# Kernel tuning notes

Hardware: AMD Instinct MI355X
Metric: run time of the kernel (lower is better)

## Reference

```python
import jax, jax.numpy as jnp
import numpy as np

B, S, P, I = 32, 64, 32, 256
NF, H, L = 4, 512, 2
OUT = 2
INITRANGE = 0.1
assert NF * I == 2 * H  # layer-2 GRU input dim equals layer-1 input dim


def setup_inputs() -> dict:
    key = jax.random.key(0)
    ks = jax.random.split(key, 12)
    u = lambda k, shape: jax.random.uniform(k, shape, jnp.float32, -INITRANGE, INITRANGE)
    return {
        "inputs": jax.random.normal(ks[0], (B, S, P, I), jnp.float32),
        "inputs_demoip": jax.random.normal(ks[1], (B, 3), jnp.float32),
        "conv_w": u(ks[2], (NF, I)),            # Conv1d(1, NF, kernel=I) == dot product
        "conv_b": u(ks[3], (NF,)),
        "conv2_w": u(ks[4], (2 * H,)),          # Conv1d(1, 1, kernel=2H) == dot product
        "conv2_b": u(ks[5], (1,)),
        "wih": u(ks[6], (L, 2, 3 * H, NF * I)),  # [layer, dir, 3H, in]
        "whh": u(ks[7], (L, 2, 3 * H, H)),
        "bih": u(ks[8], (L, 2, 3 * H)),
        "bhh": u(ks[9], (L, 2, 3 * H)),
        "lin_w": u(ks[10], (OUT, 2 * H + 3)),
        "lin_b": u(ks[11], (OUT,)),
        "batch_size": B,
    }


def _gru_dir(x, wih, whh, bih, bhh, reverse):
    """One direction of a torch-style GRU. x: [B,S,in] -> [B,S,H]."""
    gx = jnp.einsum('bsi,gi->bsg', x, wih) + bih  # precompute input gates [B,S,3H]
    if reverse:
        gx = gx[:, ::-1]
    h0 = jnp.zeros((x.shape[0], H), x.dtype)

    def step(h, gxt):
        gh = h @ whh.T + bhh
        xr, xz, xn = jnp.split(gxt, 3, axis=-1)
        hr, hz, hn = jnp.split(gh, 3, axis=-1)
        r = jax.nn.sigmoid(xr + hr)
        z = jax.nn.sigmoid(xz + hz)
        n = jnp.tanh(xn + r * hn)
        h_new = (1.0 - z) * n + z * h
        return h_new, h_new

    _, ys = jax.lax.scan(step, h0, gx.transpose(1, 0, 2))
    ys = ys.transpose(1, 0, 2)  # [B,S,H]
    if reverse:
        ys = ys[:, ::-1]
    return ys


def reference(inputs, inputs_demoip, conv_w, conv_b, conv2_w, conv2_b,
              wih, whh, bih, bhh, lin_w, lin_b, batch_size):
    # --- convolutional attention embedding (kernel spans full input -> dot product) ---
    scores = jnp.einsum('bspi,fi->bsfp', inputs, conv_w) + conv_b[None, None, :, None]
    conv_wts = jax.nn.softmax(scores, axis=-1)                    # softmax over pad dim
    vec = jnp.einsum('bsfp,bspi->bsfi', conv_wts, inputs)         # [B,S,NF,I]
    embedding = vec.reshape(batch_size, S, NF * I)                # [B,S,NF*I]

    # --- stacked bidirectional GRU (eval mode: dropout omitted) ---
    x = embedding
    for l in range(L):
        f = _gru_dir(x, wih[l, 0], whh[l, 0], bih[l, 0], bhh[l, 0], False)
        b = _gru_dir(x, wih[l, 1], whh[l, 1], bih[l, 1], bhh[l, 1], True)
        x = jnp.concatenate([f, b], axis=-1)
    states = x                                                    # [B,S,2H]

    # --- second attention (conv2 kernel spans 2H -> dot product per step) ---
    alpha = jax.nn.softmax(states @ conv2_w + conv2_b[0], axis=1)  # [B,S]
    context = jnp.einsum('bs,bsh->bh', alpha, states)              # [B,2H]

    context_v2 = jnp.concatenate([context, inputs_demoip], axis=1)  # [B,2H+3]
    out = jax.nn.softmax(context_v2 @ lin_w.T + lin_b, axis=1)      # [B,OUT]
    return out, conv_wts, states, context, alpha
```

## Files before the change

### kernel.cpp

```cpp
#include <hip/hip_runtime.h>

typedef __attribute__((ext_vector_type(8))) short s8v;
typedef __attribute__((ext_vector_type(8))) __bf16 bf8v;
typedef __attribute__((ext_vector_type(4))) float f32x4;
typedef unsigned long long ULL;

#define DEVINL __device__ __forceinline__

DEVINL unsigned short f2bf(float f) {
    unsigned int x = __float_as_uint(f);
    unsigned int r = (x + 0x7FFFu + ((x >> 16) & 1u)) >> 16;
    return (unsigned short)r;
}

DEVINL f32x4 mfma16(s8v a, s8v b, f32x4 c) {
    return __builtin_amdgcn_mfma_f32_16x16x32_bf16(
        __builtin_bit_cast(bf8v, a), __builtin_bit_cast(bf8v, b), c, 0, 0, 0);
}

typedef const __attribute__((address_space(1))) unsigned int gu32;
typedef __attribute__((address_space(3))) unsigned int lu32;
DEVINL void gload16(const void* g, unsigned int lds_off) {
    __builtin_amdgcn_global_load_lds((gu32*)g, (lu32*)(size_t)lds_off, 16, 0, 0);
}

#define WS_CTR   0
#define WS_HBUF  4096
#define WS_ZERO_BYTES 266240
#define WS_WIH   266240
#define WS_WHH   (WS_WIH + 12582912)
#define WS_EMB   (WS_WHH + 6291456)
#define WS_ST1   (WS_EMB + 4194304)
#define WS_GX    (WS_ST1 + 4194304)

__global__ __launch_bounds__(256) void k_cvt(const float* __restrict__ in,
                                             unsigned short* __restrict__ out, int n) {
    int i0 = (blockIdx.x * 256 + threadIdx.x) * 8;
    if (i0 + 8 > n) return;
    f32x4 a = *(const f32x4*)(in + i0);
    f32x4 b = *(const f32x4*)(in + i0 + 4);
    s8v o;
    o[0] = (short)f2bf(a[0]); o[1] = (short)f2bf(a[1]);
    o[2] = (short)f2bf(a[2]); o[3] = (short)f2bf(a[3]);
    o[4] = (short)f2bf(b[0]); o[5] = (short)f2bf(b[1]);
    o[6] = (short)f2bf(b[2]); o[7] = (short)f2bf(b[3]);
    *(s8v*)(out + i0) = o;
}

__global__ __launch_bounds__(256) void k_conv(const float* __restrict__ inp,
                                              const float* __restrict__ conv_w,
                                              const float* __restrict__ conv_b,
                                              float* __restrict__ wts_out,
                                              unsigned short* __restrict__ emb) {
    const int bs = blockIdx.x, tid = threadIdx.x;
    __shared__ float xs[32][260];
    __shared__ float sc[4][32];
    __shared__ float wts[4][32];
    const float* x = inp + (size_t)bs * 8192;
    {
        int p = tid >> 3, i0 = (tid & 7) * 32;
        const float* src = x + p * 256 + i0;
        float* dst = &xs[p][i0];
#pragma unroll
        for (int j = 0; j < 32; j += 4) *(f32x4*)(dst + j) = *(const f32x4*)(src + j);
    }
    __syncthreads();
    {
        int p = tid >> 3, o = tid & 7;
        float s0 = 0, s1 = 0, s2 = 0, s3 = 0;
        const float* xp = &xs[p][o * 32];
#pragma unroll
        for (int j = 0; j < 32; j += 4) {
            f32x4 v  = *(const f32x4*)(xp + j);
            f32x4 w0 = *(const f32x4*)(conv_w + o * 32 + j);
            f32x4 w1 = *(const f32x4*)(conv_w + 256 + o * 32 + j);
            f32x4 w2 = *(const f32x4*)(conv_w + 512 + o * 32 + j);
            f32x4 w3 = *(const f32x4*)(conv_w + 768 + o * 32 + j);
#pragma unroll
            for (int q = 0; q < 4; ++q) {
                s0 += v[q] * w0[q]; s1 += v[q] * w1[q];
                s2 += v[q] * w2[q]; s3 += v[q] * w3[q];
            }
        }
#pragma unroll
        for (int d = 4; d; d >>= 1) {
            s0 += __shfl_down(s0, d, 8); s1 += __shfl_down(s1, d, 8);
            s2 += __shfl_down(s2, d, 8); s3 += __shfl_down(s3, d, 8);
        }
        if (o == 0) {
            sc[0][p] = s0 + conv_b[0]; sc[1][p] = s1 + conv_b[1];
            sc[2][p] = s2 + conv_b[2]; sc[3][p] = s3 + conv_b[3];
        }
    }
    __syncthreads();
    if (tid < 4) {
        float mx = -1e30f;
        for (int p = 0; p < 32; ++p) mx = fmaxf(mx, sc[tid][p]);
        float sm = 0.f;
        for (int p = 0; p < 32; ++p) { float e = __expf(sc[tid][p] - mx); wts[tid][p] = e; sm += e; }
        float inv = 1.f / sm;
        for (int p = 0; p < 32; ++p) wts[tid][p] *= inv;
    }
    __syncthreads();
    if (tid < 128) wts_out[(size_t)bs * 128 + tid] = wts[tid >> 5][tid & 31];
    {
        float a0 = 0, a1 = 0, a2 = 0, a3 = 0;
#pragma unroll 8
        for (int p = 0; p < 32; ++p) {
            float v = xs[p][tid];
            a0 += wts[0][p] * v; a1 += wts[1][p] * v;
            a2 += wts[2][p] * v; a3 += wts[3][p] * v;
        }
        unsigned short* e = emb + (size_t)bs * 1024;
        e[tid] = f2bf(a0); e[256 + tid] = f2bf(a1);
        e[512 + tid] = f2bf(a2); e[768 + tid] = f2bf(a3);
    }
}

__global__ __launch_bounds__(256, 2) void k_gemm(const unsigned short* __restrict__ A,
                                                 const unsigned short* __restrict__ B,
                                                 const float* __restrict__ bias,
                                                 const float* __restrict__ bias2,
                                                 float* __restrict__ C,
                                                 int M, int N, int K) {
    const int bm = blockIdx.y * 128, bn = blockIdx.x * 64;
    const int tid = threadIdx.x, w = tid >> 6, l = tid & 63;
    const int wr = w >> 1, wc = w & 1;
    const int lr = l & 15, lq = l >> 4;

    __shared__ __align__(1024) unsigned short As[8192];
    __shared__ __align__(1024) unsigned short Bs[4096];
    const unsigned int AsOff = (unsigned int)(size_t)(void*)As;
    const unsigned int BsOff = (unsigned int)(size_t)(void*)Bs;

    f32x4 acc[4][2] = {};
    const int srow = tid >> 3;
    const int scol = ((tid & 7) ^ (srow & 7)) * 8;
    const unsigned int wbase = w * 1024;

    for (int k0 = 0; k0 < K; k0 += 64) {
        __syncthreads();
#pragma unroll
        for (int j = 0; j < 4; ++j)
            gload16(A + (size_t)(bm + j * 32 + srow) * K + k0 + scol,
                    AsOff + j * 4096 + wbase);
#pragma unroll
        for (int j = 0; j < 2; ++j)
            gload16(B + (size_t)(bn + j * 32 + srow) * K + k0 + scol,
                    BsOff + j * 4096 + wbase);
        asm volatile("s_waitcnt vmcnt(0)" ::: "memory");
        __syncthreads();
#pragma unroll
        for (int kk = 0; kk < 2; ++kk) {
            s8v af[4], bf_[2];
#pragma unroll
            for (int mt = 0; mt < 4; ++mt) {
                const int row = wr * 64 + mt * 16 + lr;
                const int qg = kk * 4 + lq;
                af[mt] = *(const s8v*)((const char*)As + row * 128 +
                                       ((qg ^ (row & 7)) << 4));
            }
#pragma unroll
            for (int nt = 0; nt < 2; ++nt) {
                const int row = wc * 32 + nt * 16 + lr;
                const int qg = kk * 4 + lq;
                bf_[nt] = *(const s8v*)((const char*)Bs + row * 128 +
                                        ((qg ^ (row & 7)) << 4));
            }
#pragma unroll
            for (int mt = 0; mt < 4; ++mt)
#pragma unroll
                for (int nt = 0; nt < 2; ++nt)
                    acc[mt][nt] = mfma16(af[mt], bf_[nt], acc[mt][nt]);
        }
    }
#pragma unroll
    for (int mt = 0; mt < 4; ++mt)
#pragma unroll
        for (int nt = 0; nt < 2; ++nt)
#pragma unroll
            for (int r = 0; r < 4; ++r) {
                int row = bm + wr * 64 + mt * 16 + lq * 4 + r;
                int col = bn + wc * 32 + nt * 16 + lr;
                int gg = col >> 9;
                float b2 = (gg != 2 && gg != 5) ? bias2[col] : 0.f;
                C[(size_t)row * N + col] = acc[mt][nt][r] + bias[col] + b2;
            }
}

__global__ __launch_bounds__(256, 1) void k_scan(const float* __restrict__ gx,
                                                 const unsigned short* __restrict__ whh,
                                                 const float* __restrict__ bhh,
                                                 unsigned short* __restrict__ hbuf,
                                                 unsigned int* __restrict__ flags,
                                                 float* __restrict__ st32,
                                                 unsigned short* __restrict__ st16) {
    const int blk = blockIdx.x;
    const int dir = blk >> 3, jg = blk & 7;
    const int tid = threadIdx.x;
    const int w = tid >> 6, l = tid & 63;
    const int lr = l & 15, lq = l >> 4;
    const int jb = jg * 64;
    const int mycol = jb + w * 16 + lr;

    __shared__ __align__(1024) unsigned short hs[16384];

    s8v bf[3][16];
#pragma unroll
    for (int g = 0; g < 3; ++g) {
        const unsigned short* wr =
            whh + ((size_t)dir * 1536 + g * 512 + mycol) * 512 + lq * 8;
#pragma unroll
        for (int kt = 0; kt < 16; ++kt) bf[g][kt] = *(const s8v*)(wr + kt * 32);
    }
    const float bh_n = bhh[dir * 1536 + 1024 + mycol];

    unsigned short* hb0 = hbuf + (size_t)dir * 32768;
    unsigned int* fl = flags + dir * 128;
    unsigned int* myflag = fl + jg * 16;

    float hp[2][4] = {{0.f, 0.f, 0.f, 0.f}, {0.f, 0.f, 0.f, 0.f}};

    for (int t = 0; t < 64; ++t) {
        const int s = dir ? (63 - t) : t;
        float pg[3][2][4];
#pragma unroll
        for (int g = 0; g < 3; ++g)
#pragma unroll
            for (int bt = 0; bt < 2; ++bt)
#pragma unroll
                for (int r = 0; r < 4; ++r) {
                    const int b = bt * 16 + lq * 4 + r;
                    pg[g][bt][r] = gx[(size_t)(b * 64 + s) * 3072 + dir * 1536 +
                                      g * 512 + mycol];
                }
        if (t > 0) {
            for (;;) {
                bool ok = (l >= 8) ||
                          (__hip_atomic_load(&fl[l * 16], __ATOMIC_RELAXED,
                                             __HIP_MEMORY_SCOPE_AGENT) >= (unsigned)t);
                if (__all(ok)) break;
                __builtin_amdgcn_s_sleep(1);
            }
        }
        const unsigned short* hc = hb0 + (size_t)(t & 1) * 16384;
#pragma unroll
        for (int i = 0; i < 8; ++i) {
            const int c = tid + 256 * i;
            const int row = c >> 6, inb = (c & 63) * 16;
            const ULL* hq = (const ULL*)(hc + c * 8);
            ULL d0 = __hip_atomic_load(hq, __ATOMIC_RELAXED, __HIP_MEMORY_SCOPE_AGENT);
            ULL d1 = __hip_atomic_load(hq + 1, __ATOMIC_RELAXED, __HIP_MEMORY_SCOPE_AGENT);
            char* dst = (char*)hs + row * 1024 + (inb ^ ((row & 7) << 4));
            *(ULL*)dst = d0;
            *(ULL*)(dst + 8) = d1;
        }
        __syncthreads();
        f32x4 acc[3][2] = {};
#pragma unroll
        for (int bt = 0; bt < 2; ++bt) {
            const int row = bt * 16 + lr;
            const int m = (row & 7) << 4;
#pragma unroll
            for (int kt = 0; kt < 16; ++kt) {
                s8v a = *(const s8v*)((const char*)hs + row * 1024 +
                                      ((kt * 64 + lq * 16) ^ m));
                acc[0][bt] = mfma16(a, bf[0][kt], acc[0][bt]);
                acc[1][bt] = mfma16(a, bf[1][kt], acc[1][bt]);
                acc[2][bt] = mfma16(a, bf[2][kt], acc[2][bt]);
            }
        }
        unsigned short* hnw = hb0 + (size_t)((t + 1) & 1) * 16384;
        float hnew[2][4];
#pragma unroll
        for (int bt = 0; bt < 2; ++bt)
#pragma unroll
            for (int r = 0; r < 4; ++r) {
                const int b = bt * 16 + lq * 4 + r;
                float r_ = __builtin_amdgcn_rcpf(
                    1.f + __expf(-(pg[0][bt][r] + acc[0][bt][r])));
                float z_ = __builtin_amdgcn_rcpf(
                    1.f + __expf(-(pg[1][bt][r] + acc[1][bt][r])));
                float q = pg[2][bt][r] + r_ * (acc[2][bt][r] + bh_n);
                q = fminf(fmaxf(q, -15.f), 15.f);
                float e = __expf(2.f * q);
                float n_ = (e - 1.f) * __builtin_amdgcn_rcpf(e + 1.f);
                float h = (1.f - z_) * n_ + z_ * hp[bt][r];
                hp[bt][r] = h;
                hnew[bt][r] = h;
                __hip_atomic_store(&hnw[b * 512 + mycol], f2bf(h), __ATOMIC_RELAXED,
                                   __HIP_MEMORY_SCOPE_AGENT);
            }
        __syncthreads();
        if (tid == 0 && t < 63)
            __hip_atomic_store(myflag, (unsigned)(t + 1), __ATOMIC_RELAXED,
                               __HIP_MEMORY_SCOPE_AGENT);
#pragma unroll
        for (int bt = 0; bt < 2; ++bt)
#pragma unroll
            for (int r = 0; r < 4; ++r) {
                const int b = bt * 16 + lq * 4 + r;
                const size_t so = (size_t)(b * 64 + s) * 1024 + dir * 512 + mycol;
                if (st32) st32[so] = hnew[bt][r];
                if (st16) st16[so] = f2bf(hnew[bt][r]);
            }
    }
}

__global__ __launch_bounds__(256) void k_finale(const float* __restrict__ states,
                                                const float* __restrict__ conv2_w,
                                                const float* __restrict__ conv2_b,
                                                const float* __restrict__ demoip,
                                                const float* __restrict__ lin_w,
                                                const float* __restrict__ lin_b,
                                                float* __restrict__ out,
                                                float* __restrict__ context,
                                                float* __restrict__ alpha) {
    const int b = blockIdx.x, tid = threadIdx.x, w = tid >> 6, l = tid & 63;
    __shared__ float dots[64], al[64], ctx[1024], lg[2];
    const float* st = states + (size_t)b * 65536;
    for (int si = 0; si < 16; ++si) {
        int s = w * 16 + si;
        const float* row = st + s * 1024;
        float sum = 0.f;
        for (int i = l; i < 1024; i += 64) sum += row[i] * conv2_w[i];
#pragma unroll
        for (int m = 32; m; m >>= 1) sum += __shfl_xor(sum, m, 64);
        if (l == 0) dots[s] = sum + conv2_b[0];
    }
    __syncthreads();
    if (w == 0) {
        float v = dots[l];
        float mx = v;
#pragma unroll
        for (int m = 32; m; m >>= 1) mx = fmaxf(mx, __shfl_xor(mx, m, 64));
        float e = __expf(v - mx);
        float sm = e;
#pragma unroll
        for (int m = 32; m; m >>= 1) sm += __shfl_xor(sm, m, 64);
        float a = e / sm;
        al[l] = a;
        alpha[b * 64 + l] = a;
    }
    __syncthreads();
    for (int h = tid; h < 1024; h += 256) {
        float c = 0.f;
#pragma unroll 8
        for (int s = 0; s < 64; ++s) c += al[s] * st[s * 1024 + h];
        ctx[h] = c;
        context[b * 1024 + h] = c;
    }
    __syncthreads();
    if (w < 2) {
        const float* lw = lin_w + w * 1027;
        float sum = 0.f;
        for (int i = l; i < 1024; i += 64) sum += ctx[i] * lw[i];
#pragma unroll
        for (int m = 32; m; m >>= 1) sum += __shfl_xor(sum, m, 64);
        if (l == 0) {
            sum += lw[1024] * demoip[b * 3] + lw[1025] * demoip[b * 3 + 1] +
                   lw[1026] * demoip[b * 3 + 2] + lin_b[w];
            lg[w] = sum;
        }
    }
    __syncthreads();
    if (tid == 0) {
        float m = fmaxf(lg[0], lg[1]);
        float e0 = __expf(lg[0] - m), e1 = __expf(lg[1] - m);
        float inv = 1.f / (e0 + e1);
        out[b * 2 + 0] = e0 * inv;
        out[b * 2 + 1] = e1 * inv;
    }
}

extern "C" void kernel_launch(void* const* d_in, const int* in_sizes, int n_in,
                              void* d_out, int out_size, void* d_ws, size_t ws_size,
                              hipStream_t stream) {
    const float* inputs  = (const float*)d_in[0];
    const float* demoip  = (const float*)d_in[1];
    const float* conv_w  = (const float*)d_in[2];
    const float* conv_b  = (const float*)d_in[3];
    const float* conv2_w = (const float*)d_in[4];
    const float* conv2_b = (const float*)d_in[5];
    const float* wih     = (const float*)d_in[6];
    const float* whh     = (const float*)d_in[7];
    const float* bih     = (const float*)d_in[8];
    const float* bhh     = (const float*)d_in[9];
    const float* lin_w   = (const float*)d_in[10];
    const float* lin_b   = (const float*)d_in[11];

    char* ws = (char*)d_ws;
    unsigned int* ctrs    = (unsigned int*)(ws + WS_CTR);
    unsigned short* hbuf  = (unsigned short*)(ws + WS_HBUF);
    unsigned short* wih16 = (unsigned short*)(ws + WS_WIH);
    unsigned short* whh16 = (unsigned short*)(ws + WS_WHH);
    unsigned short* emb16 = (unsigned short*)(ws + WS_EMB);
    unsigned short* st116 = (unsigned short*)(ws + WS_ST1);
    float* gxbuf          = (float*)(ws + WS_GX);

    float* out_out    = (float*)d_out;
    float* wts_out    = out_out + 64;
    float* states_out = out_out + 262208;
    float* ctx_out    = out_out + 2359360;
    float* alpha_out  = out_out + 2392128;

    hipMemsetAsync(ws, 0, WS_ZERO_BYTES, stream);
    k_cvt<<<3072, 256, 0, stream>>>(wih, wih16, 6291456);
    k_cvt<<<1536, 256, 0, stream>>>(whh, whh16, 3145728);
    k_conv<<<2048, 256, 0, stream>>>(inputs, conv_w, conv_b, wts_out, emb16);
    k_gemm<<<dim3(48, 16), 256, 0, stream>>>(emb16, wih16, bih, bhh, gxbuf,
                                             2048, 3072, 1024);
    k_scan<<<16, 256, 0, stream>>>(gxbuf, whh16, bhh, hbuf, ctrs, nullptr, st116);
    k_gemm<<<dim3(48, 16), 256, 0, stream>>>(st116, wih16 + 3145728, bih + 3072,
                                             bhh + 3072, gxbuf, 2048, 3072, 1024);
    k_scan<<<16, 256, 0, stream>>>(gxbuf, whh16 + 1572864, bhh + 3072, hbuf + 65536,
                                   ctrs + 256, states_out, nullptr);
    k_finale<<<32, 256, 0, stream>>>(states_out, conv2_w, conv2_b, demoip, lin_w, lin_b,
                                     out_out, ctx_out, alpha_out);
}
```

Measured before the change: 834.1 us.

## Fuse both GRU layers' GEMMs and scans into one persistent producer-consumer kernel

Replaces the four separate GEMM and scan launches with one persistent kernel of 256 blocks. Sixteen blocks run the recurrent scan and the other 240 compute input-gate GEMM tiles, publishing per-column-tile completion counters. Each scan block starts as soon as the gate columns it needs are complete, rather than waiting for the whole GEMM kernel to finish, and the layer-2 GEMM starts once a done counter shows every layer-1 scan block has finished. The per-step flag wait is also changed so one wave polls and then releases the block through a barrier. The design depends on all 256 blocks being resident at once and on relaxed atomic loads and stores for cross-block visibility, which adds deadlock and memory-ordering risk.

```diff
diff --git a/kernel.cpp b/kernel.cpp
--- a/kernel.cpp
+++ b/kernel.cpp
@@ -24,10 +24,24 @@
     __builtin_amdgcn_global_load_lds((gu32*)g, (lu32*)(size_t)lds_off, 16, 0, 0);
 }
 
+#define AGENT __HIP_MEMORY_SCOPE_AGENT
+DEVINL unsigned int aload(const unsigned int* p) {
+    return __hip_atomic_load(p, __ATOMIC_RELAXED, AGENT);
+}
+DEVINL float aloadf(const float* p) {
+    return __hip_atomic_load(p, __ATOMIC_RELAXED, AGENT);
+}
+DEVINL ULL aload8(const ULL* p) {
+    return __hip_atomic_load(p, __ATOMIC_RELAXED, AGENT);
+}
+
 #define WS_CTR   0
-#define WS_HBUF  4096
-#define WS_ZERO_BYTES 266240
-#define WS_WIH   266240
+#define WS_GC1   4096
+#define WS_GC2   7168
+#define WS_DONE  10240
+#define WS_HBUF  10496
+#define WS_ZERO_BYTES 272640
+#define WS_WIH   272640
 #define WS_WHH   (WS_WIH + 12582912)
 #define WS_EMB   (WS_WHH + 6291456)
 #define WS_ST1   (WS_EMB + 4194304)
@@ -117,19 +131,19 @@
     }
 }
 
-__global__ __launch_bounds__(256, 2) void k_gemm(const unsigned short* __restrict__ A,
-                                                 const unsigned short* __restrict__ B,
-                                                 const float* __restrict__ bias,
-                                                 const float* __restrict__ bias2,
-                                                 float* __restrict__ C,
-                                                 int M, int N, int K) {
-    const int bm = blockIdx.y * 128, bn = blockIdx.x * 64;
-    const int tid = threadIdx.x, w = tid >> 6, l = tid & 63;
+DEVINL void do_tile(const unsigned short* __restrict__ A,
+                    const unsigned short* __restrict__ B,
+                    const float* __restrict__ bias,
+                    const float* __restrict__ bias2,
+                    float* __restrict__ C,
+                    unsigned int* __restrict__ gcnt,
+                    int id, int tid, char* smem) {
+    const int bm = (id & 15) * 128, bn = (id >> 4) * 64;
+    const int w = tid >> 6, l = tid & 63;
     const int wr = w >> 1, wc = w & 1;
     const int lr = l & 15, lq = l >> 4;
-
-    __shared__ __align__(1024) unsigned short As[8192];
-    __shared__ __align__(1024) unsigned short Bs[4096];
+    unsigned short* As = (unsigned short*)smem;
+    unsigned short* Bs = (unsigned short*)(smem + 16384);
     const unsigned int AsOff = (unsigned int)(size_t)(void*)As;
     const unsigned int BsOff = (unsigned int)(size_t)(void*)Bs;
 
@@ -138,15 +152,15 @@
     const int scol = ((tid & 7) ^ (srow & 7)) * 8;
     const unsigned int wbase = w * 1024;
 
-    for (int k0 = 0; k0 < K; k0 += 64) {
+    for (int k0 = 0; k0 < 1024; k0 += 64) {
         __syncthreads();
 #pragma unroll
         for (int j = 0; j < 4; ++j)
-            gload16(A + (size_t)(bm + j * 32 + srow) * K + k0 + scol,
+            gload16(A + (size_t)(bm + j * 32 + srow) * 1024 + k0 + scol,
                     AsOff + j * 4096 + wbase);
 #pragma unroll
         for (int j = 0; j < 2; ++j)
-            gload16(B + (size_t)(bn + j * 32 + srow) * K + k0 + scol,
+            gload16(B + (size_t)(bn + j * 32 + srow) * 1024 + k0 + scol,
                     BsOff + j * 4096 + wbase);
         asm volatile("s_waitcnt vmcnt(0)" ::: "memory");
         __syncthreads();
@@ -184,39 +198,49 @@
                 int col = bn + wc * 32 + nt * 16 + lr;
                 int gg = col >> 9;
                 float b2 = (gg != 2 && gg != 5) ? bias2[col] : 0.f;
-                C[(size_t)row * N + col] = acc[mt][nt][r] + bias[col] + b2;
-            }
-}
-
-__global__ __launch_bounds__(256, 1) void k_scan(const float* __restrict__ gx,
-                                                 const unsigned short* __restrict__ whh,
-                                                 const float* __restrict__ bhh,
-                                                 unsigned short* __restrict__ hbuf,
-                                                 unsigned int* __restrict__ flags,
-                                                 float* __restrict__ st32,
-                                                 unsigned short* __restrict__ st16) {
-    const int blk = blockIdx.x;
-    const int dir = blk >> 3, jg = blk & 7;
-    const int tid = threadIdx.x;
+                float v = acc[mt][nt][r] + bias[col] + b2;
+                __hip_atomic_store(&C[(size_t)row * 3072 + col], v,
+                                   __ATOMIC_RELAXED, AGENT);
+            }
+    __syncthreads();
+    if (tid == 0)
+        (void)__hip_atomic_fetch_add(&gcnt[(id >> 4) * 16], 1u, __ATOMIC_RELAXED, AGENT);
+}
+
+DEVINL void scan_layer(int dir, int jg, int tid,
+                       const float* __restrict__ gx,
+                       const unsigned short* __restrict__ whh_l,
+                       const float* __restrict__ bhh_l,
+                       unsigned short* __restrict__ hbuf_l,
+                       unsigned int* __restrict__ fl_base,
+                       unsigned int* __restrict__ gcnt,
+                       float* __restrict__ st32,
+                       unsigned short* __restrict__ st16,
+                       unsigned short* __restrict__ hs) {
     const int w = tid >> 6, l = tid & 63;
     const int lr = l & 15, lq = l >> 4;
     const int jb = jg * 64;
     const int mycol = jb + w * 16 + lr;
 
-    __shared__ __align__(1024) unsigned short hs[16384];
+    for (;;) {
+        bool ok = true;
+        if (l < 3) ok = aload(&gcnt[(dir * 24 + l * 8 + jg) * 16]) >= 16u;
+        if (__all(ok)) break;
+        __builtin_amdgcn_s_sleep(4);
+    }
 
     s8v bf[3][16];
 #pragma unroll
     for (int g = 0; g < 3; ++g) {
         const unsigned short* wr =
-            whh + ((size_t)dir * 1536 + g * 512 + mycol) * 512 + lq * 8;
+            whh_l + ((size_t)dir * 1536 + g * 512 + mycol) * 512 + lq * 8;
 #pragma unroll
         for (int kt = 0; kt < 16; ++kt) bf[g][kt] = *(const s8v*)(wr + kt * 32);
     }
-    const float bh_n = bhh[dir * 1536 + 1024 + mycol];
-
-    unsigned short* hb0 = hbuf + (size_t)dir * 32768;
-    unsigned int* fl = flags + dir * 128;
+    const float bh_n = bhh_l[dir * 1536 + 1024 + mycol];
+
+    unsigned short* hb0 = hbuf_l + (size_t)dir * 32768;
+    unsigned int* fl = fl_base + dir * 128;
     unsigned int* myflag = fl + jg * 16;
 
     float hp[2][4] = {{0.f, 0.f, 0.f, 0.f}, {0.f, 0.f, 0.f, 0.f}};
@@ -231,17 +255,14 @@
 #pragma unroll
                 for (int r = 0; r < 4; ++r) {
                     const int b = bt * 16 + lq * 4 + r;
-                    pg[g][bt][r] = gx[(size_t)(b * 64 + s) * 3072 + dir * 1536 +
-                                      g * 512 + mycol];
+                    pg[g][bt][r] = aloadf(&gx[(size_t)(b * 64 + s) * 3072 +
+                                              dir * 1536 + g * 512 + mycol]);
                 }
         if (t > 0) {
-            for (;;) {
-                bool ok = (l >= 8) ||
-                          (__hip_atomic_load(&fl[l * 16], __ATOMIC_RELAXED,
-                                             __HIP_MEMORY_SCOPE_AGENT) >= (unsigned)t);
-                if (__all(ok)) break;
-                __builtin_amdgcn_s_sleep(1);
-            }
+            if (w == 0 && l < 8) {
+                while (aload(&fl[l * 16]) < (unsigned)t) __builtin_amdgcn_s_sleep(1);
+            }
+            __syncthreads();
         }
         const unsigned short* hc = hb0 + (size_t)(t & 1) * 16384;
 #pragma unroll
@@ -249,8 +270,8 @@
             const int c = tid + 256 * i;
             const int row = c >> 6, inb = (c & 63) * 16;
             const ULL* hq = (const ULL*)(hc + c * 8);
-            ULL d0 = __hip_atomic_load(hq, __ATOMIC_RELAXED, __HIP_MEMORY_SCOPE_AGENT);
-            ULL d1 = __hip_atomic_load(hq + 1, __ATOMIC_RELAXED, __HIP_MEMORY_SCOPE_AGENT);
+            ULL d0 = aload8(hq);
+            ULL d1 = aload8(hq + 1);
             char* dst = (char*)hs + row * 1024 + (inb ^ ((row & 7) << 4));
             *(ULL*)dst = d0;
             *(ULL*)(dst + 8) = d1;
@@ -289,12 +310,11 @@
                 hp[bt][r] = h;
                 hnew[bt][r] = h;
                 __hip_atomic_store(&hnw[b * 512 + mycol], f2bf(h), __ATOMIC_RELAXED,
-                                   __HIP_MEMORY_SCOPE_AGENT);
+                                   AGENT);
             }
         __syncthreads();
         if (tid == 0 && t < 63)
-            __hip_atomic_store(myflag, (unsigned)(t + 1), __ATOMIC_RELAXED,
-                               __HIP_MEMORY_SCOPE_AGENT);
+            __hip_atomic_store(myflag, (unsigned)(t + 1), __ATOMIC_RELAXED, AGENT);
 #pragma unroll
         for (int bt = 0; bt < 2; ++bt)
 #pragma unroll
@@ -302,8 +322,46 @@
                 const int b = bt * 16 + lq * 4 + r;
                 const size_t so = (size_t)(b * 64 + s) * 1024 + dir * 512 + mycol;
                 if (st32) st32[so] = hnew[bt][r];
-                if (st16) st16[so] = f2bf(hnew[bt][r]);
-            }
+                if (st16)
+                    __hip_atomic_store(&st16[so], f2bf(hnew[bt][r]), __ATOMIC_RELAXED,
+                                       AGENT);
+            }
+    }
+}
+
+__global__ __launch_bounds__(256, 1) void k_mega(
+    const unsigned short* __restrict__ emb16,
+    const unsigned short* __restrict__ wih16,
+    const float* __restrict__ bih,
+    const float* __restrict__ bhh,
+    float* __restrict__ gx,
+    const unsigned short* __restrict__ whh16,
+    unsigned short* __restrict__ st116,
+    float* __restrict__ states_out,
+    unsigned short* __restrict__ hbuf,
+    unsigned int* __restrict__ flags,
+    unsigned int* __restrict__ gc1,
+    unsigned int* __restrict__ gc2,
+    unsigned int* __restrict__ done) {
+    __shared__ __align__(1024) char smem[32768];
+    const int blk = blockIdx.x, tid = threadIdx.x;
+    if (blk < 16) {
+        const int dir = blk >> 3, jg = blk & 7;
+        scan_layer(dir, jg, tid, gx, whh16, bhh, hbuf, flags, gc1,
+                   nullptr, st116, (unsigned short*)smem);
+        __syncthreads();
+        if (tid == 0)
+            (void)__hip_atomic_fetch_add(done, 1u, __ATOMIC_RELAXED, AGENT);
+        scan_layer(dir, jg, tid, gx, whh16 + 1572864, bhh + 3072, hbuf + 65536,
+                   flags + 256, gc2, states_out, nullptr, (unsigned short*)smem);
+    } else {
+        const int wid = blk - 16;
+        for (int id = wid; id < 768; id += 240)
+            do_tile(emb16, wih16, bih, bhh, gx, gc1, id, tid, smem);
+        while (aload(done) < 16u) __builtin_amdgcn_s_sleep(16);
+        for (int id = wid; id < 768; id += 240)
+            do_tile(st116, wih16 + 3145728, bih + 3072, bhh + 3072, gx, gc2, id, tid,
+                    smem);
     }
 }
 
@@ -390,7 +448,10 @@
     const float* lin_b   = (const float*)d_in[11];
 
     char* ws = (char*)d_ws;
-    unsigned int* ctrs    = (unsigned int*)(ws + WS_CTR);
+    unsigned int* flags   = (unsigned int*)(ws + WS_CTR);
+    unsigned int* gc1     = (unsigned int*)(ws + WS_GC1);
+    unsigned int* gc2     = (unsigned int*)(ws + WS_GC2);
+    unsigned int* done    = (unsigned int*)(ws + WS_DONE);
     unsigned short* hbuf  = (unsigned short*)(ws + WS_HBUF);
     unsigned short* wih16 = (unsigned short*)(ws + WS_WIH);
     unsigned short* whh16 = (unsigned short*)(ws + WS_WHH);
@@ -408,13 +469,8 @@
     k_cvt<<<3072, 256, 0, stream>>>(wih, wih16, 6291456);
     k_cvt<<<1536, 256, 0, stream>>>(whh, whh16, 3145728);
     k_conv<<<2048, 256, 0, stream>>>(inputs, conv_w, conv_b, wts_out, emb16);
-    k_gemm<<<dim3(48, 16), 256, 0, stream>>>(emb16, wih16, bih, bhh, gxbuf,
-                                             2048, 3072, 1024);
-    k_scan<<<16, 256, 0, stream>>>(gxbuf, whh16, bhh, hbuf, ctrs, nullptr, st116);
-    k_gemm<<<dim3(48, 16), 256, 0, stream>>>(st116, wih16 + 3145728, bih + 3072,
-                                             bhh + 3072, gxbuf, 2048, 3072, 1024);
-    k_scan<<<16, 256, 0, stream>>>(gxbuf, whh16 + 1572864, bhh + 3072, hbuf + 65536,
-                                   ctrs + 256, states_out, nullptr);
+    k_mega<<<256, 256, 0, stream>>>(emb16, wih16, bih, bhh, gxbuf, whh16, st116,
+                                    states_out, hbuf, flags, gc1, gc2, done);
     k_finale<<<32, 256, 0, stream>>>(states_out, conv2_w, conv2_b, demoip, lin_w, lin_b,
                                      out_out, ctx_out, alpha_out);
 }
```

New measurement: 1.002 ms. 1.2x slower.

## Merge weight conversion, conv and flag reset into one prep kernel; simplify scan wait

Applied to the files above, without the earlier changes.

Folds the two bf16 weight-conversion launches, the conv attention kernel and the workspace memset into a single k_prep launch. Block 0 of that launch zeroes the flag counters. In the scan, a single wave now spins on the flags and then releases the block with a barrier, and the step-0 h-load and MFMA work are skipped because h is zero. This cuts launch and memset overhead and per-step polling traffic, at the cost of an extra barrier per step. The hbuf region is no longer zeroed, which is safe only because the t==0 path never reads it.

```diff
diff --git a/kernel.cpp b/kernel.cpp
--- a/kernel.cpp
+++ b/kernel.cpp
@@ -24,35 +24,48 @@
     __builtin_amdgcn_global_load_lds((gu32*)g, (lu32*)(size_t)lds_off, 16, 0, 0);
 }
 
+#define AGENT __HIP_MEMORY_SCOPE_AGENT
+
 #define WS_CTR   0
 #define WS_HBUF  4096
-#define WS_ZERO_BYTES 266240
 #define WS_WIH   266240
 #define WS_WHH   (WS_WIH + 12582912)
 #define WS_EMB   (WS_WHH + 6291456)
 #define WS_ST1   (WS_EMB + 4194304)
 #define WS_GX    (WS_ST1 + 4194304)
 
-__global__ __launch_bounds__(256) void k_cvt(const float* __restrict__ in,
-                                             unsigned short* __restrict__ out, int n) {
-    int i0 = (blockIdx.x * 256 + threadIdx.x) * 8;
-    if (i0 + 8 > n) return;
-    f32x4 a = *(const f32x4*)(in + i0);
-    f32x4 b = *(const f32x4*)(in + i0 + 4);
-    s8v o;
-    o[0] = (short)f2bf(a[0]); o[1] = (short)f2bf(a[1]);
-    o[2] = (short)f2bf(a[2]); o[3] = (short)f2bf(a[3]);
-    o[4] = (short)f2bf(b[0]); o[5] = (short)f2bf(b[1]);
-    o[6] = (short)f2bf(b[2]); o[7] = (short)f2bf(b[3]);
-    *(s8v*)(out + i0) = o;
-}
-
-__global__ __launch_bounds__(256) void k_conv(const float* __restrict__ inp,
+__global__ __launch_bounds__(256) void k_prep(const float* __restrict__ inp,
                                               const float* __restrict__ conv_w,
                                               const float* __restrict__ conv_b,
                                               float* __restrict__ wts_out,
-                                              unsigned short* __restrict__ emb) {
-    const int bs = blockIdx.x, tid = threadIdx.x;
+                                              unsigned short* __restrict__ emb,
+                                              const float* __restrict__ wih,
+                                              unsigned short* __restrict__ wih16,
+                                              const float* __restrict__ whh,
+                                              unsigned short* __restrict__ whh16,
+                                              unsigned int* __restrict__ flagz) {
+    const int bid = blockIdx.x, tid = threadIdx.x;
+    if (bid >= 2048) {
+        const float* src;
+        unsigned short* dst;
+        int i0;
+        if (bid < 5120) { src = wih; dst = wih16; i0 = ((bid - 2048) * 256 + tid) * 8; }
+        else            { src = whh; dst = whh16; i0 = ((bid - 5120) * 256 + tid) * 8; }
+        f32x4 a = *(const f32x4*)(src + i0);
+        f32x4 b = *(const f32x4*)(src + i0 + 4);
+        s8v o;
+        o[0] = (short)f2bf(a[0]); o[1] = (short)f2bf(a[1]);
+        o[2] = (short)f2bf(a[2]); o[3] = (short)f2bf(a[3]);
+        o[4] = (short)f2bf(b[0]); o[5] = (short)f2bf(b[1]);
+        o[6] = (short)f2bf(b[2]); o[7] = (short)f2bf(b[3]);
+        *(s8v*)(dst + i0) = o;
+        return;
+    }
+    const int bs = bid;
+    if (bs == 0) {
+        for (int i = tid; i < 1024; i += 256)
+            __hip_atomic_store(&flagz[i], 0u, __ATOMIC_RELAXED, AGENT);
+    }
     __shared__ float xs[32][260];
     __shared__ float sc[4][32];
     __shared__ float wts[4][32];
@@ -234,40 +247,39 @@
                     pg[g][bt][r] = gx[(size_t)(b * 64 + s) * 3072 + dir * 1536 +
                                       g * 512 + mycol];
                 }
+        f32x4 acc[3][2] = {};
         if (t > 0) {
-            for (;;) {
-                bool ok = (l >= 8) ||
-                          (__hip_atomic_load(&fl[l * 16], __ATOMIC_RELAXED,
-                                             __HIP_MEMORY_SCOPE_AGENT) >= (unsigned)t);
-                if (__all(ok)) break;
-                __builtin_amdgcn_s_sleep(1);
-            }
-        }
-        const unsigned short* hc = hb0 + (size_t)(t & 1) * 16384;
-#pragma unroll
-        for (int i = 0; i < 8; ++i) {
-            const int c = tid + 256 * i;
-            const int row = c >> 6, inb = (c & 63) * 16;
-            const ULL* hq = (const ULL*)(hc + c * 8);
-            ULL d0 = __hip_atomic_load(hq, __ATOMIC_RELAXED, __HIP_MEMORY_SCOPE_AGENT);
-            ULL d1 = __hip_atomic_load(hq + 1, __ATOMIC_RELAXED, __HIP_MEMORY_SCOPE_AGENT);
-            char* dst = (char*)hs + row * 1024 + (inb ^ ((row & 7) << 4));
-            *(ULL*)dst = d0;
-            *(ULL*)(dst + 8) = d1;
-        }
-        __syncthreads();
-        f32x4 acc[3][2] = {};
-#pragma unroll
-        for (int bt = 0; bt < 2; ++bt) {
-            const int row = bt * 16 + lr;
-            const int m = (row & 7) << 4;
-#pragma unroll
-            for (int kt = 0; kt < 16; ++kt) {
-                s8v a = *(const s8v*)((const char*)hs + row * 1024 +
-                                      ((kt * 64 + lq * 16) ^ m));
-                acc[0][bt] = mfma16(a, bf[0][kt], acc[0][bt]);
-                acc[1][bt] = mfma16(a, bf[1][kt], acc[1][bt]);
-                acc[2][bt] = mfma16(a, bf[2][kt], acc[2][bt]);
+            if (w == 0 && l < 8) {
+                while (__hip_atomic_load(&fl[l * 16], __ATOMIC_RELAXED, AGENT) <
+                       (unsigned)t)
+                    __builtin_amdgcn_s_sleep(1);
+            }
+            __syncthreads();
+            const unsigned short* hc = hb0 + (size_t)(t & 1) * 16384;
+#pragma unroll
+            for (int i = 0; i < 8; ++i) {
+                const int c = tid + 256 * i;
+                const int row = c >> 6, inb = (c & 63) * 16;
+                const ULL* hq = (const ULL*)(hc + c * 8);
+                ULL d0 = __hip_atomic_load(hq, __ATOMIC_RELAXED, AGENT);
+                ULL d1 = __hip_atomic_load(hq + 1, __ATOMIC_RELAXED, AGENT);
+                char* dst = (char*)hs + row * 1024 + (inb ^ ((row & 7) << 4));
+                *(ULL*)dst = d0;
+                *(ULL*)(dst + 8) = d1;
+            }
+            __syncthreads();
+#pragma unroll
+            for (int bt = 0; bt < 2; ++bt) {
+                const int row = bt * 16 + lr;
+                const int m = (row & 7) << 4;
+#pragma unroll
+                for (int kt = 0; kt < 16; ++kt) {
+                    s8v a = *(const s8v*)((const char*)hs + row * 1024 +
+                                          ((kt * 64 + lq * 16) ^ m));
+                    acc[0][bt] = mfma16(a, bf[0][kt], acc[0][bt]);
+                    acc[1][bt] = mfma16(a, bf[1][kt], acc[1][bt]);
+                    acc[2][bt] = mfma16(a, bf[2][kt], acc[2][bt]);
+                }
             }
         }
         unsigned short* hnw = hb0 + (size_t)((t + 1) & 1) * 16384;
@@ -289,12 +301,11 @@
                 hp[bt][r] = h;
                 hnew[bt][r] = h;
                 __hip_atomic_store(&hnw[b * 512 + mycol], f2bf(h), __ATOMIC_RELAXED,
-                                   __HIP_MEMORY_SCOPE_AGENT);
+                                   AGENT);
             }
         __syncthreads();
         if (tid == 0 && t < 63)
-            __hip_atomic_store(myflag, (unsigned)(t + 1), __ATOMIC_RELAXED,
-                               __HIP_MEMORY_SCOPE_AGENT);
+            __hip_atomic_store(myflag, (unsigned)(t + 1), __ATOMIC_RELAXED, AGENT);
 #pragma unroll
         for (int bt = 0; bt < 2; ++bt)
 #pragma unroll
@@ -404,10 +415,8 @@
     float* ctx_out    = out_out + 2359360;
     float* alpha_out  = out_out + 2392128;
 
-    hipMemsetAsync(ws, 0, WS_ZERO_BYTES, stream);
-    k_cvt<<<3072, 256, 0, stream>>>(wih, wih16, 6291456);
-    k_cvt<<<1536, 256, 0, stream>>>(whh, whh16, 3145728);
-    k_conv<<<2048, 256, 0, stream>>>(inputs, conv_w, conv_b, wts_out, emb16);
+    k_prep<<<6656, 256, 0, stream>>>(inputs, conv_w, conv_b, wts_out, emb16,
+                                     wih, wih16, whh, whh16, ctrs);
     k_gemm<<<dim3(48, 16), 256, 0, stream>>>(emb16, wih16, bih, bhh, gxbuf,
                                              2048, 3072, 1024);
     k_scan<<<16, 256, 0, stream>>>(gxbuf, whh16, bhh, hbuf, ctrs, nullptr, st116);
```

Result: faster. 801.0 us (median of 2 runs) (-4.0%).
